# Performance work log

Hardware: AMD Instinct MI355X
Metric: run time of the kernel (lower is better)

The kernel has to match this reference:

```python
import jax, jax.numpy as jnp
import numpy as np

B, L, D = 8, 2048, 1152  # batch, frames, d_model (multiple of headdim=36)


def setup_inputs() -> dict:
    key = jax.random.key(0)
    k1, k2, k3 = jax.random.split(key, 3)
    hidden_states = jax.random.normal(k1, (B, L, D), dtype=jnp.float32)
    Wq = jax.random.normal(k2, (D, D), dtype=jnp.float32) * 0.02  # xavier-ish, gain 0.1
    Wk = jax.random.normal(k3, (D, D), dtype=jnp.float32) * 0.02
    log_temperature = jnp.zeros((), dtype=jnp.float32)
    boundary_bias = jnp.asarray(-1.0, dtype=jnp.float32)
    mask = jnp.ones((B, L), dtype=bool)
    return dict(hidden_states=hidden_states, Wq=Wq, Wk=Wk,
                log_temperature=log_temperature, boundary_bias=boundary_bias,
                mask=mask)


def _normalize(x, eps=1e-12):
    # F.normalize: x / max(||x||, eps)
    n = jnp.sqrt(jnp.sum(x * x, axis=-1, keepdims=True))
    return x / jnp.maximum(n, eps)


def reference(hidden_states, Wq, Wk, log_temperature, boundary_bias, mask):
    Bb, Ll, Dd = hidden_states.shape
    # ---- RoutingModule (eval mode: argmax boundary decision) ----
    q = jnp.einsum('bld,ed->ble', hidden_states[:, :-1], Wq)
    k = jnp.einsum('bld,ed->ble', hidden_states[:, 1:], Wk)
    cos_sim = jnp.sum(_normalize(q) * _normalize(k), axis=-1)          # (B, L-1)
    temperature = jnp.clip(jnp.exp(log_temperature), 0.1, 10.0)
    bl = (1.0 - cos_sim) * temperature + boundary_bias                 # dissimilarity logits
    bl = jnp.pad(bl, ((0, 0), (1, 0)), constant_values=10.0)           # force boundary at t=0
    logits = jnp.stack([-bl, bl], axis=-1)                             # (B, L, 2)
    boundary_prob = jax.nn.softmax(logits, axis=-1)
    boundary_mask = (bl > 0) & mask                                    # argmax == 1  <=>  bl > 0
    selected_probs = jnp.where(boundary_mask, boundary_prob[..., 1], boundary_prob[..., 0])

    # ---- ChunkLayer: stable-sort boundary frames to the front (static M = L pad) ----
    token_idx = jnp.arange(Ll)[None, :] + (~boundary_mask).astype(jnp.int32) * Ll
    sorted_idx = jnp.argsort(token_idx, axis=1)                        # (B, L)
    chunked = jnp.take_along_axis(hidden_states, sorted_idx[..., None], axis=1)  # (B, L, D)

    # ---- DeChunkLayer: EMA over chunks  h_t = (1-p_t) h_{t-1} + p_t x_t,  h_0 = x_0 ----
    p = jnp.clip(boundary_prob[..., 1], 1e-4, 1.0 - 1e-4)
    p_c = jnp.take_along_axis(p, sorted_idx, axis=1)                   # (B, L)
    a = (1.0 - p_c).at[:, 0].set(0.0)[..., None]                       # (B, L, 1)
    b = (p_c[..., None] * chunked).at[:, 0].set(chunked[:, 0])         # (B, L, D)

    def combine(c1, c2):
        a1, b1 = c1
        a2, b2 = c2
        return a1 * a2, a2 * b1 + b2

    _, ema = jax.lax.associative_scan(combine, (a, b), axis=1)         # (B, L, D)

    # scatter-expand: position t reads chunk (cumsum(boundary) - 1)
    chunk_idx = jnp.clip(jnp.cumsum(boundary_mask.astype(jnp.int32), axis=1) - 1, 0, Ll - 1)
    expanded = jnp.take_along_axis(ema, chunk_idx[..., None], axis=1)  # (B, L, D)

    # STE confidence gate: forward multiplies by 1, backward routes grad to selected_probs
    ste = 1.0 + selected_probs - jax.lax.stop_gradient(selected_probs)
    return expanded * ste[..., None]
```

## Files before the change

### kernel.cpp

```cpp
#include <hip/hip_runtime.h>
#include <hip/hip_bf16.h>
#include <cstdint>
#include <cstddef>

#define Bc 8
#define Lc 2048
#define Dc 1152
#define STRIDE 2080
#define G 8
#define NCHUNK 18

#define WCV_OFF   0u
#define PART_OFF  10616832u
#define BL_OFF    17694720u
#define PV_OFF    17760256u
#define BPOS_OFF  17826816u
#define NB_OFF    17893376u

using bf16x8 = __attribute__((ext_vector_type(8))) short;
using f32x4  = __attribute__((ext_vector_type(4))) float;
#define MFMA(a, b, c) __builtin_amdgcn_mfma_f32_16x16x32_bf16(a, b, c, 0, 0, 0)

__device__ __forceinline__ void gld16(const void* g, void* l) {
    __builtin_amdgcn_global_load_lds(
        (const __attribute__((address_space(1))) void*)(g),
        (__attribute__((address_space(3))) void*)(l), 16, 0, 0);
}

__device__ __forceinline__ unsigned short bf_hi(float x) {
    __hip_bfloat16 h = __float2bfloat16(x);
    return *reinterpret_cast<unsigned short*>(&h);
}
__device__ __forceinline__ float bf_f(unsigned short u) {
    __hip_bfloat16 h; *reinterpret_cast<unsigned short*>(&h) = u;
    return __bfloat162float(h);
}

__global__ __launch_bounds__(256) void k0_convert(
    const float* __restrict__ H, const float* __restrict__ Wq,
    const float* __restrict__ Wk, char* __restrict__ Hcv, char* __restrict__ Wcv)
{
    int idx = blockIdx.x * 256 + threadIdx.x;
    if (idx >= (16384 + 2304) * 144) return;
    int cchunk = idx & 3;
    int ks = (idx >> 2) % 36;
    int row = idx / 144;
    const float* src;
    char* dst;
    if (row < 16384) {
        src = H + (size_t)row * Dc;
        dst = Hcv + ((size_t)row * 36 + ks) * 128;
    } else {
        int e = row - 16384;
        src = (e < Dc) ? (Wq + (size_t)e * Dc) : (Wk + (size_t)(e - Dc) * Dc);
        dst = Wcv + ((size_t)e * 36 + ks) * 128;
    }
    const float* s = src + ks * 32 + cchunk * 8;
    unsigned int hw0 = 0, hw1 = 0, hw2 = 0, hw3 = 0;
    unsigned int lw0 = 0, lw1 = 0, lw2 = 0, lw3 = 0;
    #define CV(i, HW, LW, SH)                                                  \
    {                                                                          \
        float x = s[i];                                                        \
        unsigned short h = bf_hi(x);                                           \
        unsigned short lo = bf_hi(x - bf_f(h));                                \
        HW |= ((unsigned int)h) << (SH);                                       \
        LW |= ((unsigned int)lo) << (SH);                                      \
    }
    CV(0, hw0, lw0, 0) CV(1, hw0, lw0, 16) CV(2, hw1, lw1, 0) CV(3, hw1, lw1, 16)
    CV(4, hw2, lw2, 0) CV(5, hw2, lw2, 16) CV(6, hw3, lw3, 0) CV(7, hw3, lw3, 16)
    #undef CV
    uint4 hv; hv.x = hw0; hv.y = hw1; hv.z = hw2; hv.w = hw3;
    uint4 lv; lv.x = lw0; lv.y = lw1; lv.z = lw2; lv.w = lw3;
    *(uint4*)(dst + cchunk * 16) = hv;
    *(uint4*)(dst + 64 + cchunk * 16) = lv;
}

__global__ __launch_bounds__(256, 2) void k1_mfma(
    const char* __restrict__ Hcv, const char* __restrict__ Wcv,
    float* __restrict__ partial)
{
    __shared__ __align__(16) char LdsB[32896];
    const int tid = threadIdx.x;
    const int bid = blockIdx.x;
    const int x = bid & 7;
    const int r = bid >> 3;
    const int g = x + 8 * (r / 18);
    const int j = r % 18;
    const int batch = g >> 4;
    const int mt = g & 15;
    const int t0 = 1 + mt * 128;
    const int rowbase = batch * Lc + t0 - 1;
    const int rowmax = batch * Lc + (Lc - 1);

    const char *hp0, *hpt, *wp0;
    {
        int row = tid >> 3;
        int ch = (tid & 7) ^ (row & 7);
        hp0 = Hcv + (size_t)(rowbase + row) * 4608 + (ch << 4);
        int gr2 = rowbase + 128; if (gr2 > rowmax) gr2 = rowmax;
        hpt = Hcv + (size_t)gr2 * 4608 + ((tid & 7) << 4);
        wp0 = Wcv + (size_t)(j * 64 + row) * 4608 + (ch << 4);
    }

    const int l = tid & 63;
    const int w = tid >> 6;
    const int rl = l & 15;
    const int c = l >> 4;

    const int sA = c ^ (rl & 7);
    const int sB = c ^ ((rl + 1) & 7);
    const int offAh = rl * 128 + (sA << 4);
    const int offAl = rl * 128 + ((sA ^ 4) << 4);
    const int offBh = (rl + 1) * 128 + (sB << 4);
    const int offBl = (rl + 1) * 128 + ((sB ^ 4) << 4);
    const char* Wb = LdsB + 16512;

    f32x4 q00{0,0,0,0}, q01{0,0,0,0}, q02{0,0,0,0}, q03{0,0,0,0};
    f32x4 q10{0,0,0,0}, q11{0,0,0,0}, q12{0,0,0,0}, q13{0,0,0,0};
    f32x4 k00{0,0,0,0}, k01{0,0,0,0}, k02{0,0,0,0}, k03{0,0,0,0};
    f32x4 k10{0,0,0,0}, k11{0,0,0,0}, k12{0,0,0,0}, k13{0,0,0,0};

    for (int ks = 0; ks < 36; ++ks) {
        gld16(hp0,           LdsB + tid * 16);
        gld16(hp0 + 147456,  LdsB + (tid + 256) * 16);
        gld16(hp0 + 294912,  LdsB + (tid + 512) * 16);
        gld16(hp0 + 442368,  LdsB + (tid + 768) * 16);
        if (tid < 8) gld16(hpt, LdsB + (1024 + tid) * 16);
        gld16(wp0,           LdsB + 16512 + tid * 16);
        gld16(wp0 + 147456,  LdsB + 16512 + (tid + 256) * 16);
        gld16(wp0 + 5308416, LdsB + 16512 + (tid + 512) * 16);
        gld16(wp0 + 5455872, LdsB + 16512 + (tid + 768) * 16);
        hp0 += 128; hpt += 128; wp0 += 128;
        __syncthreads();

        const char* hm0 = LdsB + (2 * w) * 2048;
        const char* hm1 = LdsB + (2 * w + 1) * 2048;
        bf16x8 a0h = *(const bf16x8*)(hm0 + offAh);
        bf16x8 a0l = *(const bf16x8*)(hm0 + offAl);
        bf16x8 b0h = *(const bf16x8*)(hm0 + offBh);
        bf16x8 b0l = *(const bf16x8*)(hm0 + offBl);
        bf16x8 a1h = *(const bf16x8*)(hm1 + offAh);
        bf16x8 a1l = *(const bf16x8*)(hm1 + offAl);
        bf16x8 b1h = *(const bf16x8*)(hm1 + offBh);
        bf16x8 b1l = *(const bf16x8*)(hm1 + offBl);

        #define FSTEP(f, QA0, QA1, KA0, KA1)                                   \
        {                                                                      \
            const char* wqb = Wb + (f) * 2048;                                 \
            bf16x8 wh = *(const bf16x8*)(wqb + offAh);                         \
            bf16x8 wl = *(const bf16x8*)(wqb + offAl);                         \
            QA0 = MFMA(a0h, wh, QA0); QA0 = MFMA(a0h, wl, QA0);                \
            QA0 = MFMA(a0l, wh, QA0);                                          \
            QA1 = MFMA(a1h, wh, QA1); QA1 = MFMA(a1h, wl, QA1);                \
            QA1 = MFMA(a1l, wh, QA1);                                          \
            const char* wkb = Wb + 8192 + (f) * 2048;                          \
            bf16x8 vh = *(const bf16x8*)(wkb + offAh);                         \
            bf16x8 vl = *(const bf16x8*)(wkb + offAl);                         \
            KA0 = MFMA(b0h, vh, KA0); KA0 = MFMA(b0h, vl, KA0);                \
            KA0 = MFMA(b0l, vh, KA0);                                          \
            KA1 = MFMA(b1h, vh, KA1); KA1 = MFMA(b1h, vl, KA1);                \
            KA1 = MFMA(b1l, vh, KA1);                                          \
            __builtin_amdgcn_sched_barrier(0);                                 \
        }
        FSTEP(0, q00, q10, k00, k10)
        FSTEP(1, q01, q11, k01, k11)
        FSTEP(2, q02, q12, k02, k12)
        FSTEP(3, q03, q13, k03, k13)
        #undef FSTEP
        __syncthreads();
    }

    #define EMIT(QA, QB, QC, QD, KA, KB, KC, KD, TROW)                         \
    {                                                                          \
        float qq = (QA)*(QA) + (QB)*(QB) + (QC)*(QC) + (QD)*(QD);              \
        float kk = (KA)*(KA) + (KB)*(KB) + (KC)*(KC) + (KD)*(KD);              \
        float qk = (QA)*(KA) + (QB)*(KB) + (QC)*(KC) + (QD)*(KD);              \
        qq += __shfl_xor(qq, 1, 64); qq += __shfl_xor(qq, 2, 64);              \
        qq += __shfl_xor(qq, 4, 64); qq += __shfl_xor(qq, 8, 64);              \
        kk += __shfl_xor(kk, 1, 64); kk += __shfl_xor(kk, 2, 64);              \
        kk += __shfl_xor(kk, 4, 64); kk += __shfl_xor(kk, 8, 64);              \
        qk += __shfl_xor(qk, 1, 64); qk += __shfl_xor(qk, 2, 64);              \
        qk += __shfl_xor(qk, 4, 64); qk += __shfl_xor(qk, 8, 64);              \
        if (rl == 0) {                                                         \
            int t = t0 + (TROW);                                               \
            if (t < Lc) {                                                      \
                size_t pidx = (((size_t)j * Bc + batch) * Lc + t) * 3;         \
                partial[pidx] = qq; partial[pidx + 1] = kk;                    \
                partial[pidx + 2] = qk;                                        \
            }                                                                  \
        }                                                                      \
    }
    EMIT(q00[0], q01[0], q02[0], q03[0], k00[0], k01[0], k02[0], k03[0], 32*w + c*4 + 0)
    EMIT(q00[1], q01[1], q02[1], q03[1], k00[1], k01[1], k02[1], k03[1], 32*w + c*4 + 1)
    EMIT(q00[2], q01[2], q02[2], q03[2], k00[2], k01[2], k02[2], k03[2], 32*w + c*4 + 2)
    EMIT(q00[3], q01[3], q02[3], q03[3], k00[3], k01[3], k02[3], k03[3], 32*w + c*4 + 3)
    EMIT(q10[0], q11[0], q12[0], q13[0], k10[0], k11[0], k12[0], k13[0], 32*w + 16 + c*4 + 0)
    EMIT(q10[1], q11[1], q12[1], q13[1], k10[1], k11[1], k12[1], k13[1], 32*w + 16 + c*4 + 1)
    EMIT(q10[2], q11[2], q12[2], q13[2], k10[2], k11[2], k12[2], k13[2], 32*w + 16 + c*4 + 2)
    EMIT(q10[3], q11[3], q12[3], q13[3], k10[3], k11[3], k12[3], k13[3], 32*w + 16 + c*4 + 3)
    #undef EMIT
}

__global__ __launch_bounds__(256) void k1b_reduce(
    const float* __restrict__ partial, const float* __restrict__ ltemp,
    const float* __restrict__ bbias, float* __restrict__ bl_out)
{
    int idx = blockIdx.x * 256 + threadIdx.x;
    if (idx >= Bc * Lc) return;
    int t = idx & (Lc - 1);
    if (t == 0) return;
    float qq = 0.f, kk = 0.f, qk = 0.f;
    #pragma unroll
    for (int cn = 0; cn < NCHUNK; ++cn) {
        size_t p = ((size_t)cn * Bc * Lc + idx) * 3;
        qq += partial[p];
        kk += partial[p + 1];
        qk += partial[p + 2];
    }
    float T = expf(ltemp[0]);
    T = fminf(fmaxf(T, 0.1f), 10.0f);
    float den = fmaxf(sqrtf(qq), 1e-12f) * fmaxf(sqrtf(kk), 1e-12f);
    bl_out[idx] = (1.0f - qk / den) * T + bbias[0];
}

__global__ __launch_bounds__(256) void k2_boundary(
    const float* __restrict__ bl_in, const int* __restrict__ mask,
    float* __restrict__ pv, int* __restrict__ bpos, int* __restrict__ nb)
{
    int b = blockIdx.x;
    int tid = threadIdx.x;
    const float* blb = bl_in + b * Lc;
    const int* mb = mask + b * Lc;

    float blv[8]; int f[8];
    int t0 = tid * 8;
    int s = 0;
    #pragma unroll
    for (int i = 0; i < 8; ++i) {
        int t = t0 + i;
        float v = (t == 0) ? 10.0f : blb[t];
        blv[i] = v;
        f[i] = (v > 0.0f && mb[t] != 0) ? 1 : 0;
        s += f[i];
    }
    int lane = tid & 63, wv = tid >> 6;
    int sc = s;
    #pragma unroll
    for (int off = 1; off < 64; off <<= 1) {
        int o = __shfl_up(sc, off, 64);
        if (lane >= off) sc += o;
    }
    __shared__ int wsums[4];
    if (lane == 63) wsums[wv] = sc;
    __syncthreads();
    int woff = 0;
    #pragma unroll
    for (int w2 = 0; w2 < 4; ++w2) woff += (w2 < wv) ? wsums[w2] : 0;
    int excl = woff + sc - s;
    int total = wsums[0] + wsums[1] + wsums[2] + wsums[3];

    float* pvb = pv + b * STRIDE;
    int* bpb = bpos + b * STRIDE;
    int r = excl;
    #pragma unroll
    for (int i = 0; i < 8; ++i) {
        if (f[i]) {
            int t = t0 + i;
            float p;
            if (t == 0) {
                p = 1.0f;
            } else {
                p = 1.0f / (1.0f + expf(-2.0f * blv[i]));
                p = fminf(fmaxf(p, 1e-4f), 1.0f - 1e-4f);
            }
            bpb[r] = t;
            pvb[r] = p;
            r += 1;
        }
    }
    if (tid == 0) nb[b] = total;
    for (int q = total + tid; q < STRIDE; q += 256) { bpb[q] = Lc; pvb[q] = 0.0f; }
}

__global__ __launch_bounds__(128) void k3_ema(
    const float* __restrict__ H, const float* __restrict__ pv,
    const int* __restrict__ bpos, const int* __restrict__ nb,
    float* __restrict__ out)
{
    int b = blockIdx.x;
    int ch = blockIdx.y * 128 + threadIdx.x;
    const float* Hb = H + (size_t)b * Lc * Dc + ch;
    float* Ob = out + (size_t)b * Lc * Dc + ch;
    const float* pvb = pv + b * STRIDE;
    const int* bpb = bpos + b * STRIDE;
    int n = nb[b];
    int ng = (n + G - 1) / G;

    float xA[G], pA[G]; int tA[G + 1];
    #pragma unroll
    for (int i = 0; i < G; ++i) {
        int t = bpb[i];
        tA[i] = t;
        pA[i] = pvb[i];
        xA[i] = (t < Lc) ? Hb[(size_t)t * Dc] : 0.0f;
    }
    tA[G] = bpb[G];

    float h = 0.0f;
    for (int g = 0; g < ng; ++g) {
        int nbase = (g + 1) * G;
        float xB[G], pB[G]; int tB[G + 1];
        #pragma unroll
        for (int i = 0; i < G; ++i) {
            int t = bpb[nbase + i];
            tB[i] = t;
            pB[i] = pvb[nbase + i];
            xB[i] = (t < Lc) ? Hb[(size_t)t * Dc] : 0.0f;
        }
        tB[G] = bpb[nbase + G];
        #pragma unroll
        for (int i = 0; i < G; ++i) {
            h = (1.0f - pA[i]) * h + pA[i] * xA[i];
            int te = tA[i + 1];
            for (int tt = tA[i]; tt < te; ++tt) Ob[(size_t)tt * Dc] = h;
        }
        #pragma unroll
        for (int i = 0; i < G; ++i) { xA[i] = xB[i]; pA[i] = pB[i]; tA[i] = tB[i]; }
        tA[G] = tB[G];
    }
}

extern "C" void kernel_launch(void* const* d_in, const int* in_sizes, int n_in,
                              void* d_out, int out_size, void* d_ws, size_t ws_size,
                              hipStream_t stream)
{
    const float* H  = (const float*)d_in[0];
    const float* Wq = (const float*)d_in[1];
    const float* Wk = (const float*)d_in[2];
    const float* lt = (const float*)d_in[3];
    const float* bb = (const float*)d_in[4];
    const int* mask = (const int*)d_in[5];
    float* out = (float*)d_out;

    char* ws = (char*)d_ws;
    char*  Hcv  = (char*)d_out;
    char*  Wcv  = ws + WCV_OFF;
    float* part = (float*)(ws + PART_OFF);
    float* bl   = (float*)(ws + BL_OFF);
    float* pv   = (float*)(ws + PV_OFF);
    int*   bpos = (int*)(ws + BPOS_OFF);
    int*   nbp  = (int*)(ws + NB_OFF);

    hipLaunchKernelGGL(k0_convert, dim3(((16384 + 2304) * 144 + 255) / 256),
                       dim3(256), 0, stream, H, Wq, Wk, Hcv, Wcv);
    hipLaunchKernelGGL(k1_mfma, dim3(NCHUNK * 128), dim3(256), 0, stream,
                       Hcv, Wcv, part);
    hipLaunchKernelGGL(k1b_reduce, dim3((Bc * Lc + 255) / 256), dim3(256), 0, stream,
                       part, lt, bb, bl);
    hipLaunchKernelGGL(k2_boundary, dim3(Bc), dim3(256), 0, stream,
                       bl, mask, pv, bpos, nbp);
    hipLaunchKernelGGL(k3_ema, dim3(Bc, 9), dim3(128), 0, stream,
                       H, pv, bpos, nbp, out);
}
```

Measured before the change: 364.9 us.

## Double-buffer LDS tiles in the MFMA projection kernel to overlap loads with compute

The shared-memory staging area in k1_mfma grows to two buffers. The global-to-LDS loads for the next k-step are now issued before the MFMAs run on the current buffer, so the previous load→barrier→compute serialization is replaced by a prefetch pipeline. The cost is doubled LDS per block (about 64 KB). With two blocks per CU this may still fit the CU's LDS, but it tightens the occupancy margin.

```diff
diff --git a/kernel.cpp b/kernel.cpp
--- a/kernel.cpp
+++ b/kernel.cpp
@@ -79,7 +79,7 @@
     const char* __restrict__ Hcv, const char* __restrict__ Wcv,
     float* __restrict__ partial)
 {
-    __shared__ __align__(16) char LdsB[32896];
+    __shared__ __align__(16) char LdsB[65792];
     const int tid = threadIdx.x;
     const int bid = blockIdx.x;
     const int x = bid & 7;
@@ -113,28 +113,37 @@
     const int offAl = rl * 128 + ((sA ^ 4) << 4);
     const int offBh = (rl + 1) * 128 + (sB << 4);
     const int offBl = (rl + 1) * 128 + ((sB ^ 4) << 4);
-    const char* Wb = LdsB + 16512;
 
     f32x4 q00{0,0,0,0}, q01{0,0,0,0}, q02{0,0,0,0}, q03{0,0,0,0};
     f32x4 q10{0,0,0,0}, q11{0,0,0,0}, q12{0,0,0,0}, q13{0,0,0,0};
     f32x4 k00{0,0,0,0}, k01{0,0,0,0}, k02{0,0,0,0}, k03{0,0,0,0};
     f32x4 k10{0,0,0,0}, k11{0,0,0,0}, k12{0,0,0,0}, k13{0,0,0,0};
 
+    #define STAGE(PAR)                                                         \
+    {                                                                          \
+        char* B = LdsB + (PAR) * 32896;                                        \
+        gld16(hp0,           B + tid * 16);                                    \
+        gld16(hp0 + 147456,  B + (tid + 256) * 16);                            \
+        gld16(hp0 + 294912,  B + (tid + 512) * 16);                            \
+        gld16(hp0 + 442368,  B + (tid + 768) * 16);                            \
+        if (tid < 8) gld16(hpt, B + (1024 + tid) * 16);                        \
+        gld16(wp0,           B + 16512 + tid * 16);                            \
+        gld16(wp0 + 147456,  B + 16512 + (tid + 256) * 16);                    \
+        gld16(wp0 + 5308416, B + 16512 + (tid + 512) * 16);                    \
+        gld16(wp0 + 5455872, B + 16512 + (tid + 768) * 16);                    \
+        hp0 += 128; hpt += 128; wp0 += 128;                                    \
+    }
+
+    STAGE(0)
+    __syncthreads();
+
     for (int ks = 0; ks < 36; ++ks) {
-        gld16(hp0,           LdsB + tid * 16);
-        gld16(hp0 + 147456,  LdsB + (tid + 256) * 16);
-        gld16(hp0 + 294912,  LdsB + (tid + 512) * 16);
-        gld16(hp0 + 442368,  LdsB + (tid + 768) * 16);
-        if (tid < 8) gld16(hpt, LdsB + (1024 + tid) * 16);
-        gld16(wp0,           LdsB + 16512 + tid * 16);
-        gld16(wp0 + 147456,  LdsB + 16512 + (tid + 256) * 16);
-        gld16(wp0 + 5308416, LdsB + 16512 + (tid + 512) * 16);
-        gld16(wp0 + 5455872, LdsB + 16512 + (tid + 768) * 16);
-        hp0 += 128; hpt += 128; wp0 += 128;
-        __syncthreads();
-
-        const char* hm0 = LdsB + (2 * w) * 2048;
-        const char* hm1 = LdsB + (2 * w + 1) * 2048;
+        if (ks < 35) STAGE((ks + 1) & 1)
+
+        const char* buf = LdsB + (ks & 1) * 32896;
+        const char* Wb  = buf + 16512;
+        const char* hm0 = buf + (2 * w) * 2048;
+        const char* hm1 = buf + (2 * w + 1) * 2048;
         bf16x8 a0h = *(const bf16x8*)(hm0 + offAh);
         bf16x8 a0l = *(const bf16x8*)(hm0 + offAl);
         bf16x8 b0h = *(const bf16x8*)(hm0 + offBh);
@@ -169,6 +178,7 @@
         #undef FSTEP
         __syncthreads();
     }
+    #undef STAGE
 
     #define EMIT(QA, QB, QC, QD, KA, KB, KC, KD, TROW)                         \
     {                                                                          \
```

Measured after the change: 371.3 us. Within noise of the previous version (+1.7%).
